# Kernel optimization log

Measured on AMD Instinct MI355X. Metric: run time of the kernel, lower is better.

## Reference

```python
import jax, jax.numpy as jnp
import numpy as np


def _segsum(x):
    """Stable segment-sum. x: (..., l) -> (..., l, l) lower-triangular sums."""
    l = x.shape[-1]
    cs = jnp.cumsum(x, axis=-1)
    seg = cs[..., :, None] - cs[..., None, :]
    mask = jnp.tril(jnp.ones((l, l), dtype=bool))
    return jnp.where(mask, seg, -jnp.inf)


def setup_inputs() -> dict:
    key = jax.random.key(0)
    kx, ka, kb, kc = jax.random.split(key, 4)
    b, s, h, p, n = 4, 8192, 32, 64, 16
    X = jax.random.normal(kx, (b, s, h, p), dtype=jnp.float32)
    # negative A for realistic decaying SSM dynamics / numerical safety
    A = -jnp.abs(jax.random.normal(ka, (b, s, h), dtype=jnp.float32)) * 0.5
    B = jax.random.normal(kb, (b, s, h, n), dtype=jnp.float32)
    C = jax.random.normal(kc, (b, s, h, n), dtype=jnp.float32)
    return {"X": X, "A": A, "B": B, "C": C, "block_len": 64}


def reference(X, A, B, C, block_len):
    b, s, h, p = X.shape
    n = B.shape[-1]
    c = s // block_len
    l = block_len
    # chunk: (b, c, l, ...)
    Xb = X.reshape(b, c, l, h, p)
    Bb = B.reshape(b, c, l, h, n)
    Cb = C.reshape(b, c, l, h, n)
    Ab = A.reshape(b, c, l, h).transpose(0, 3, 1, 2)  # (b, h, c, l)
    A_cumsum = jnp.cumsum(Ab, axis=-1)                # (b, h, c, l)

    # 1) intra-chunk (diagonal) output
    L = jnp.exp(_segsum(Ab))                          # (b, h, c, l, l)
    Y_diag = jnp.einsum("bclhn,bcshn,bhcls,bcshp->bclhp", Cb, Bb, L, Xb)

    # 2) intra-chunk states (chunk-final state contribution)
    decay_states = jnp.exp(A_cumsum[..., -1:] - A_cumsum)   # (b, h, c, l)
    states = jnp.einsum("bclhn,bhcl,bclhp->bchpn", Bb, decay_states, Xb)

    # 3) inter-chunk recurrence (zero initial states)
    A_last = A_cumsum[..., -1]                        # (b, h, c)
    decay_chunk = jnp.exp(_segsum(jnp.pad(A_last, ((0, 0), (0, 0), (1, 0)))))  # (b,h,c+1,c+1)
    states = jnp.concatenate([jnp.zeros_like(states[:, :1]), states], axis=1)  # (b,c+1,h,p,n)
    new_states = jnp.einsum("bhzc,bchpn->bzhpn", decay_chunk, states)
    states = new_states[:, :-1]                       # states entering each chunk

    # 4) state -> output (off-diagonal)
    state_decay_out = jnp.exp(A_cumsum)               # (b, h, c, l)
    Y_off = jnp.einsum("bclhn,bchpn,bhcl->bclhp", Cb, states, state_decay_out)

    Y = (Y_diag + Y_off).reshape(b, s, h, p)
    return Y
```

## Files before the change

kernel.cpp:

```cpp
#include <hip/hip_runtime.h>

#define BB 4
#define SS 8192
#define HH 32
#define PP 64
#define NN 16
#define LL 64
#define CC 128
#define SEG 4
#define NSEG (CC / SEG)
#define NCHAIN (BB * HH)
#define NSEGT (NCHAIN * NSEG)
#define NCHT (NCHAIN * CC)

typedef __attribute__((ext_vector_type(8))) short bf16x8;
typedef __attribute__((ext_vector_type(4))) short bf16x4;
typedef __attribute__((ext_vector_type(4))) float f32x4;

__device__ inline short f2bf(float f) {
    unsigned u = __builtin_bit_cast(unsigned, f);
    u = (u + 0x7FFFu + ((u >> 16) & 1u)) >> 16;
    return (short)u;
}

__global__ __launch_bounds__(256) void k1_carries(
    const float* __restrict__ X, const float* __restrict__ A,
    const float* __restrict__ B, float* __restrict__ carry,
    float* __restrict__ segd, float* __restrict__ ploc,
    float* __restrict__ dsum)
{
    int seg = blockIdx.x;
    int chain = seg >> 5;
    int kseg = seg & (NSEG - 1);
    int h = chain & (HH - 1);
    int b = chain >> 5;
    int tid = threadIdx.x;
    int w = tid >> 6, l = tid & 63, g = l >> 4, lr = l & 15;

    __shared__ float Bs[2][LL][17];
    __shared__ float csL[2][LL];
    __shared__ float wls[2][LL];

    float P[4] = {0.f, 0.f, 0.f, 0.f};
    float asum = 0.f;
    float xr[16]; float4 br; float ar = 0.f;

    int c0 = kseg * SEG;
    int pnoff = (16 * w + lr) * NN + 4 * g;

    auto LOADS = [&](int c) {
        size_t row0 = (size_t)b * SS + (size_t)c * LL;
        const float* Xp = X + (row0 * HH + h) * PP;
        const float* Bp = B + (row0 * HH + h) * NN;
        const float* Ap = A + row0 * HH + h;
#pragma unroll
        for (int kt = 0; kt < 2; ++kt)
#pragma unroll
            for (int e = 0; e < 8; ++e)
                xr[kt * 8 + e] = Xp[(size_t)(kt * 32 + g * 8 + e) * (HH * PP) + 16 * w + lr];
        br = *(const float4*)(Bp + (size_t)(tid >> 2) * (HH * NN) + (tid & 3) * 4);
        if (tid < 64) ar = Ap[(size_t)tid * HH];
    };

    auto WRITE = [&](int q1) {
        if (tid < 64) {
            float x = ar;
#pragma unroll
            for (int d = 1; d < 64; d <<= 1) {
                float t = __shfl_up(x, d, 64);
                if (tid >= d) x += t;
            }
            csL[q1][tid] = x;
            float al2 = __shfl(x, 63, 64);
            wls[q1][tid] = __expf(al2 - x);
        }
        int r = tid >> 2, qq = tid & 3;
        Bs[q1][r][qq * 4 + 0] = br.x;
        Bs[q1][r][qq * 4 + 1] = br.y;
        Bs[q1][r][qq * 4 + 2] = br.z;
        Bs[q1][r][qq * 4 + 3] = br.w;
    };

    LOADS(c0);
    WRITE(0);
    __syncthreads();

    for (int cc = 0; cc < SEG; ++cc) {
        int q = cc & 1;
        if (cc > 0) {
            float4 pv = {P[0], P[1], P[2], P[3]};
            *(float4*)(ploc + (size_t)(chain * CC + c0 + cc) * (PP * NN) + pnoff) = pv;
            if (tid == 0) dsum[chain * CC + c0 + cc] = asum;
        }
        bf16x8 xf0, xf1;
#pragma unroll
        for (int e = 0; e < 8; ++e) { xf0[e] = f2bf(xr[e]); xf1[e] = f2bf(xr[8 + e]); }
        if (cc + 1 < SEG) LOADS(c0 + cc + 1);

        bf16x8 bt[2];
#pragma unroll
        for (int kt = 0; kt < 2; ++kt) {
            bf16x8 t;
#pragma unroll
            for (int e = 0; e < 8; ++e) {
                int ll2 = kt * 32 + g * 8 + e;
                t[e] = f2bf(Bs[q][ll2][lr] * wls[q][ll2]);
            }
            bt[kt] = t;
        }
        f32x4 st = __builtin_amdgcn_mfma_f32_16x16x32_bf16(bt[0], xf0, (f32x4)0.f, 0, 0, 0);
        st = __builtin_amdgcn_mfma_f32_16x16x32_bf16(bt[1], xf1, st, 0, 0, 0);

        float alast = csL[q][LL - 1];
        float ea = __expf(alast);
#pragma unroll
        for (int r = 0; r < 4; ++r) P[r] = ea * P[r] + st[r];
        asum += alast;

        if (cc + 1 < SEG) WRITE(q ^ 1);
        __syncthreads();
    }

    float4 pv = {P[0], P[1], P[2], P[3]};
    *(float4*)(carry + (size_t)seg * (PP * NN) + pnoff) = pv;
    if (tid == 0) segd[seg] = asum;
}

__global__ __launch_bounds__(256) void k2_scan(
    const float* __restrict__ carry, const float* __restrict__ segd,
    float* __restrict__ pin)
{
    int chain = blockIdx.x >> 2;
    int t = ((blockIdx.x & 3) << 8) + threadIdx.x;
    const float* cb = carry + (size_t)chain * NSEG * (PP * NN) + t;
    float* pb = pin + (size_t)chain * NSEG * (PP * NN) + t;
    const float* as = segd + chain * NSEG;
    float P = 0.f;
    for (int k0 = 0; k0 < NSEG; k0 += 8) {
        float s[8], av[8], o[8];
#pragma unroll
        for (int u = 0; u < 8; ++u) s[u] = cb[(size_t)(k0 + u) * (PP * NN)];
#pragma unroll
        for (int u = 0; u < 8; ++u) av[u] = as[k0 + u];
#pragma unroll
        for (int u = 0; u < 8; ++u) { o[u] = P; P = __expf(av[u]) * P + s[u]; }
#pragma unroll
        for (int u = 0; u < 8; ++u) pb[(size_t)(k0 + u) * (PP * NN)] = o[u];
    }
}

__global__ __launch_bounds__(256) void k3_y(
    const float* __restrict__ X, const float* __restrict__ A,
    const float* __restrict__ Bm, const float* __restrict__ Cm,
    const float* __restrict__ pin, const float* __restrict__ ploc,
    const float* __restrict__ dsum, float* __restrict__ Y)
{
    int blk = blockIdx.x;
    int h = blk & (HH - 1);
    int c = (blk >> 5) & (CC - 1);
    int b = blk >> 12;
    int tid = threadIdx.x;
    int w = tid >> 6, l = tid & 63, g = l >> 4, lr = l & 15;
    int chain = b * HH + h;
    int seg = chain * NSEG + (c >> 2);

    __shared__ short XTF[8 * 64 * 8];
    __shared__ short ScF[8 * 64 * 8];
    __shared__ short BsF[4 * 64 * 8];
    __shared__ short PF[4 * 64 * 8];
    __shared__ float csL[LL];

    size_t row0 = (size_t)b * SS + (size_t)c * LL;
    const float* Xp = X + (row0 * HH + h) * PP;
    const float* Bp = Bm + (row0 * HH + h) * NN;
    const float* Cp = Cm + (row0 * HH + h) * NN;
    const float* Ap = A + row0 * HH + h;
    float* Yp = Y + (row0 * HH + h) * PP;

    float xr[16];
#pragma unroll
    for (int si = 0; si < 2; ++si) {
        int k0 = si * 32 + g * 8;
#pragma unroll
        for (int e = 0; e < 8; ++e)
            xr[si * 8 + e] = Xp[(size_t)(k0 + e) * (HH * PP) + 16 * w + lr];
    }
    int r = tid >> 2, q = tid & 3;
    float4 br = *(const float4*)(Bp + (size_t)r * (HH * NN) + q * 4);
    float4 cr0 = {0,0,0,0}, cr1 = {0,0,0,0};
    if (g < 2) {
        const float* crp = Cp + (size_t)(16 * w + lr) * (HH * NN) + g * 8;
        cr0 = *(const float4*)crp;
        cr1 = *(const float4*)(crp + 4);
    }
    float ar = 0.f;
    if (tid < 64) ar = Ap[(size_t)tid * HH];
    int pnoff = (16 * w + lr) * NN + 4 * g;
    float4 pinv = *(const float4*)(pin + (size_t)seg * (PP * NN) + pnoff);
    float P4[4];
    if ((c & (SEG - 1)) == 0) {
        P4[0] = pinv.x; P4[1] = pinv.y; P4[2] = pinv.z; P4[3] = pinv.w;
    } else {
        float4 plv = *(const float4*)(ploc + (size_t)(chain * CC + c) * (PP * NN) + pnoff);
        float ed = __expf(dsum[chain * CC + c]);
        P4[0] = ed * pinv.x + plv.x;
        P4[1] = ed * pinv.y + plv.y;
        P4[2] = ed * pinv.z + plv.z;
        P4[3] = ed * pinv.w + plv.w;
    }

    ((bf16x8*)ScF)[tid] = (bf16x8)0;
    ((bf16x8*)ScF)[tid + 256] = (bf16x8)0;
    if (tid < 128)
        ((bf16x8*)PF)[(tid >> 5) * 64 + 32 + (tid & 31)] = (bf16x8)0;

#pragma unroll
    for (int si = 0; si < 2; ++si) {
        bf16x8 xb;
#pragma unroll
        for (int e = 0; e < 8; ++e) xb[e] = f2bf(xr[si * 8 + e]);
        ((bf16x8*)XTF)[tid + si * 256] = xb;
    }
    {
        int fl = (r & 15) + 16 * (q >> 1);
        int jt = r >> 4;
        bf16x4 bb = { f2bf(br.x), f2bf(br.y), f2bf(br.z), f2bf(br.w) };
        ((bf16x4*)BsF)[(jt * 64 + fl) * 2 + (q & 1)] = bb;
        int zt = tid >> 6, zu = (tid >> 1) & 31, zv = tid & 1;
        ((bf16x4*)BsF)[(zt * 64 + 32 + zu) * 2 + zv] = (bf16x4)0;
    }
#pragma unroll
    for (int rr = 0; rr < 4; ++rr) {
        int n = 4 * g + rr;
        PF[(w * 64 + (n >> 3) * 16 + lr) * 8 + (n & 7)] = f2bf(P4[rr]);
    }
    bf16x8 caw = (bf16x8)0;
    if (g < 2) {
        caw[0] = f2bf(cr0.x); caw[1] = f2bf(cr0.y);
        caw[2] = f2bf(cr0.z); caw[3] = f2bf(cr0.w);
        caw[4] = f2bf(cr1.x); caw[5] = f2bf(cr1.y);
        caw[6] = f2bf(cr1.z); caw[7] = f2bf(cr1.w);
    }
    if (tid < 64) {
        float x = ar;
#pragma unroll
        for (int d = 1; d < 64; d <<= 1) {
            float t = __shfl_up(x, d, 64);
            if (tid >= d) x += t;
        }
        csL[tid] = x;
    }
    __syncthreads();

    float cs_i[4], ei[4];
    int ib = 16 * w + 4 * g;
#pragma unroll
    for (int rr = 0; rr < 4; ++rr) { cs_i[rr] = csL[ib + rr]; ei[rr] = __expf(cs_i[rr]); }

    for (int jt = 0; jt <= w; ++jt) {
        bf16x8 bw = ((bf16x8*)BsF)[jt * 64 + l];
        f32x4 sr = __builtin_amdgcn_mfma_f32_16x16x32_bf16(caw, bw, (f32x4)0.f, 0, 0, 0);
        int j = jt * 16 + lr;
        float csj = csL[j];
        int kt2 = j >> 5;
        int flb = 16 * ((j >> 3) & 3);
#pragma unroll
        for (int rr = 0; rr < 4; ++rr) {
            int i15 = g * 4 + rr;
            int i = 16 * w + i15;
            float v = (j <= i) ? sr[rr] * __expf(cs_i[rr] - csj) : 0.f;
            ScF[((w * 2 + kt2) * 64 + i15 + flb) * 8 + (j & 7)] = f2bf(v);
        }
    }

    f32x4 acc[4];
#pragma unroll
    for (int pt = 0; pt < 4; ++pt) {
        bf16x8 pfv = ((bf16x8*)PF)[pt * 64 + l];
        acc[pt] = __builtin_amdgcn_mfma_f32_16x16x32_bf16(caw, pfv, (f32x4)0.f, 0, 0, 0);
    }
#pragma unroll
    for (int pt = 0; pt < 4; ++pt)
#pragma unroll
        for (int rr = 0; rr < 4; ++rr) acc[pt][rr] *= ei[rr];

    int kts = (w >= 2) ? 2 : 1;
    for (int kt = 0; kt < kts; ++kt) {
        bf16x8 af = ((bf16x8*)ScF)[(w * 2 + kt) * 64 + l];
#pragma unroll
        for (int pt = 0; pt < 4; ++pt) {
            bf16x8 xf = ((bf16x8*)XTF)[(kt * 4 + pt) * 64 + l];
            acc[pt] = __builtin_amdgcn_mfma_f32_16x16x32_bf16(af, xf, acc[pt], 0, 0, 0);
        }
    }

#pragma unroll
    for (int pt = 0; pt < 4; ++pt)
#pragma unroll
        for (int rr = 0; rr < 4; ++rr)
            Yp[(size_t)(16 * w + 4 * g + rr) * (HH * PP) + pt * 16 + lr] = acc[pt][rr];
}

extern "C" void kernel_launch(void* const* d_in, const int* in_sizes, int n_in,
                              void* d_out, int out_size, void* d_ws, size_t ws_size,
                              hipStream_t stream)
{
    const float* X = (const float*)d_in[0];
    const float* A = (const float*)d_in[1];
    const float* B = (const float*)d_in[2];
    const float* C = (const float*)d_in[3];
    float* Y = (float*)d_out;

    float* carry = (float*)d_ws;
    float* pin   = carry + (size_t)NSEGT * (PP * NN);
    float* ploc  = pin   + (size_t)NSEGT * (PP * NN);
    float* segd  = ploc  + (size_t)NCHT * (PP * NN);
    float* dsum  = segd  + NSEGT;

    dim3 blk(256);
    k1_carries<<<dim3(NSEGT), blk, 0, stream>>>(X, A, B, carry, segd, ploc, dsum);
    k2_scan<<<dim3(NCHAIN * 4), blk, 0, stream>>>(carry, segd, pin);
    k3_y<<<dim3(NCHT), blk, 0, stream>>>(X, A, B, C, pin, ploc, dsum, Y);
}
```

Measured before the change: 275.9 us.

## Compute per-chunk states in parallel and scan all chunks in place

Replaces the segmented carry scheme (one block per 4-chunk segment, then a segment-level scan, then local-prefix fixups in the output kernel) with one block per chunk computing its own state. A scan over all 128 chunks then runs in place on the states buffer. The output kernel reads the entering state directly and replaces the shared-memory cumsum with wave shuffles. This raises parallelism in the first kernel and simplifies the third, at the cost of a longer serial scan chain (128 steps instead of 32) and more state traffic in the scan kernel.

```diff
diff --git a/kernel.cpp b/kernel.cpp
--- a/kernel.cpp
+++ b/kernel.cpp
@@ -7,10 +7,7 @@
 #define NN 16
 #define LL 64
 #define CC 128
-#define SEG 4
-#define NSEG (CC / SEG)
 #define NCHAIN (BB * HH)
-#define NSEGT (NCHAIN * NSEG)
 #define NCHT (NCHAIN * CC)
 
 typedef __attribute__((ext_vector_type(8))) short bf16x8;
@@ -23,137 +20,10 @@
     return (short)u;
 }
 
-__global__ __launch_bounds__(256) void k1_carries(
+__global__ __launch_bounds__(256) void k1_states(
     const float* __restrict__ X, const float* __restrict__ A,
-    const float* __restrict__ B, float* __restrict__ carry,
-    float* __restrict__ segd, float* __restrict__ ploc,
-    float* __restrict__ dsum)
-{
-    int seg = blockIdx.x;
-    int chain = seg >> 5;
-    int kseg = seg & (NSEG - 1);
-    int h = chain & (HH - 1);
-    int b = chain >> 5;
-    int tid = threadIdx.x;
-    int w = tid >> 6, l = tid & 63, g = l >> 4, lr = l & 15;
-
-    __shared__ float Bs[2][LL][17];
-    __shared__ float csL[2][LL];
-    __shared__ float wls[2][LL];
-
-    float P[4] = {0.f, 0.f, 0.f, 0.f};
-    float asum = 0.f;
-    float xr[16]; float4 br; float ar = 0.f;
-
-    int c0 = kseg * SEG;
-    int pnoff = (16 * w + lr) * NN + 4 * g;
-
-    auto LOADS = [&](int c) {
-        size_t row0 = (size_t)b * SS + (size_t)c * LL;
-        const float* Xp = X + (row0 * HH + h) * PP;
-        const float* Bp = B + (row0 * HH + h) * NN;
-        const float* Ap = A + row0 * HH + h;
-#pragma unroll
-        for (int kt = 0; kt < 2; ++kt)
-#pragma unroll
-            for (int e = 0; e < 8; ++e)
-                xr[kt * 8 + e] = Xp[(size_t)(kt * 32 + g * 8 + e) * (HH * PP) + 16 * w + lr];
-        br = *(const float4*)(Bp + (size_t)(tid >> 2) * (HH * NN) + (tid & 3) * 4);
-        if (tid < 64) ar = Ap[(size_t)tid * HH];
-    };
-
-    auto WRITE = [&](int q1) {
-        if (tid < 64) {
-            float x = ar;
-#pragma unroll
-            for (int d = 1; d < 64; d <<= 1) {
-                float t = __shfl_up(x, d, 64);
-                if (tid >= d) x += t;
-            }
-            csL[q1][tid] = x;
-            float al2 = __shfl(x, 63, 64);
-            wls[q1][tid] = __expf(al2 - x);
-        }
-        int r = tid >> 2, qq = tid & 3;
-        Bs[q1][r][qq * 4 + 0] = br.x;
-        Bs[q1][r][qq * 4 + 1] = br.y;
-        Bs[q1][r][qq * 4 + 2] = br.z;
-        Bs[q1][r][qq * 4 + 3] = br.w;
-    };
-
-    LOADS(c0);
-    WRITE(0);
-    __syncthreads();
-
-    for (int cc = 0; cc < SEG; ++cc) {
-        int q = cc & 1;
-        if (cc > 0) {
-            float4 pv = {P[0], P[1], P[2], P[3]};
-            *(float4*)(ploc + (size_t)(chain * CC + c0 + cc) * (PP * NN) + pnoff) = pv;
-            if (tid == 0) dsum[chain * CC + c0 + cc] = asum;
-        }
-        bf16x8 xf0, xf1;
-#pragma unroll
-        for (int e = 0; e < 8; ++e) { xf0[e] = f2bf(xr[e]); xf1[e] = f2bf(xr[8 + e]); }
-        if (cc + 1 < SEG) LOADS(c0 + cc + 1);
-
-        bf16x8 bt[2];
-#pragma unroll
-        for (int kt = 0; kt < 2; ++kt) {
-            bf16x8 t;
-#pragma unroll
-            for (int e = 0; e < 8; ++e) {
-                int ll2 = kt * 32 + g * 8 + e;
-                t[e] = f2bf(Bs[q][ll2][lr] * wls[q][ll2]);
-            }
-            bt[kt] = t;
-        }
-        f32x4 st = __builtin_amdgcn_mfma_f32_16x16x32_bf16(bt[0], xf0, (f32x4)0.f, 0, 0, 0);
-        st = __builtin_amdgcn_mfma_f32_16x16x32_bf16(bt[1], xf1, st, 0, 0, 0);
-
-        float alast = csL[q][LL - 1];
-        float ea = __expf(alast);
-#pragma unroll
-        for (int r = 0; r < 4; ++r) P[r] = ea * P[r] + st[r];
-        asum += alast;
-
-        if (cc + 1 < SEG) WRITE(q ^ 1);
-        __syncthreads();
-    }
-
-    float4 pv = {P[0], P[1], P[2], P[3]};
-    *(float4*)(carry + (size_t)seg * (PP * NN) + pnoff) = pv;
-    if (tid == 0) segd[seg] = asum;
-}
-
-__global__ __launch_bounds__(256) void k2_scan(
-    const float* __restrict__ carry, const float* __restrict__ segd,
-    float* __restrict__ pin)
-{
-    int chain = blockIdx.x >> 2;
-    int t = ((blockIdx.x & 3) << 8) + threadIdx.x;
-    const float* cb = carry + (size_t)chain * NSEG * (PP * NN) + t;
-    float* pb = pin + (size_t)chain * NSEG * (PP * NN) + t;
-    const float* as = segd + chain * NSEG;
-    float P = 0.f;
-    for (int k0 = 0; k0 < NSEG; k0 += 8) {
-        float s[8], av[8], o[8];
-#pragma unroll
-        for (int u = 0; u < 8; ++u) s[u] = cb[(size_t)(k0 + u) * (PP * NN)];
-#pragma unroll
-        for (int u = 0; u < 8; ++u) av[u] = as[k0 + u];
-#pragma unroll
-        for (int u = 0; u < 8; ++u) { o[u] = P; P = __expf(av[u]) * P + s[u]; }
-#pragma unroll
-        for (int u = 0; u < 8; ++u) pb[(size_t)(k0 + u) * (PP * NN)] = o[u];
-    }
-}
-
-__global__ __launch_bounds__(256) void k3_y(
-    const float* __restrict__ X, const float* __restrict__ A,
-    const float* __restrict__ Bm, const float* __restrict__ Cm,
-    const float* __restrict__ pin, const float* __restrict__ ploc,
-    const float* __restrict__ dsum, float* __restrict__ Y)
+    const float* __restrict__ B, float* __restrict__ states,
+    float* __restrict__ alast_g)
 {
     int blk = blockIdx.x;
     int h = blk & (HH - 1);
@@ -162,13 +32,96 @@
     int tid = threadIdx.x;
     int w = tid >> 6, l = tid & 63, g = l >> 4, lr = l & 15;
     int chain = b * HH + h;
-    int seg = chain * NSEG + (c >> 2);
+
+    __shared__ float Bs[LL][17];
+
+    size_t row0 = (size_t)b * SS + (size_t)c * LL;
+    const float* Xp = X + (row0 * HH + h) * PP;
+    const float* Bp = B + (row0 * HH + h) * NN;
+    const float* Ap = A + row0 * HH + h;
+
+    float av = Ap[(size_t)l * HH];
+    int r = tid >> 2, q = tid & 3;
+    float4 br = *(const float4*)(Bp + (size_t)r * (HH * NN) + q * 4);
+    float xr[16];
+#pragma unroll
+    for (int kt = 0; kt < 2; ++kt)
+#pragma unroll
+        for (int e = 0; e < 8; ++e)
+            xr[kt * 8 + e] = Xp[(size_t)(kt * 32 + g * 8 + e) * (HH * PP) + 16 * w + lr];
+
+    float x = av;
+#pragma unroll
+    for (int d = 1; d < 64; d <<= 1) {
+        float t = __shfl_up(x, d, 64);
+        if (l >= d) x += t;
+    }
+    float alast = __shfl(x, 63, 64);
+
+    float wlr = __expf(alast - __shfl(x, r & 63, 64));
+    Bs[r][q * 4 + 0] = br.x * wlr;
+    Bs[r][q * 4 + 1] = br.y * wlr;
+    Bs[r][q * 4 + 2] = br.z * wlr;
+    Bs[r][q * 4 + 3] = br.w * wlr;
+    __syncthreads();
+
+    bf16x8 bt[2], xf[2];
+#pragma unroll
+    for (int kt = 0; kt < 2; ++kt)
+#pragma unroll
+        for (int e = 0; e < 8; ++e) {
+            int row = kt * 32 + g * 8 + e;
+            bt[kt][e] = f2bf(Bs[row][lr]);
+            xf[kt][e] = f2bf(xr[kt * 8 + e]);
+        }
+    f32x4 st = __builtin_amdgcn_mfma_f32_16x16x32_bf16(bt[0], xf[0], (f32x4)0.f, 0, 0, 0);
+    st = __builtin_amdgcn_mfma_f32_16x16x32_bf16(bt[1], xf[1], st, 0, 0, 0);
+
+    float4 pv = {st[0], st[1], st[2], st[3]};
+    *(float4*)(states + (size_t)(chain * CC + c) * (PP * NN) + (16 * w + lr) * NN + 4 * g) = pv;
+    if (tid == 0) alast_g[chain * CC + c] = alast;
+}
+
+__global__ __launch_bounds__(256) void k2_scan(
+    float* __restrict__ states, const float* __restrict__ alast_g)
+{
+    int chain = blockIdx.x >> 2;
+    int t = ((blockIdx.x & 3) << 8) + threadIdx.x;
+    __shared__ float eal[CC];
+    if (threadIdx.x < CC)
+        eal[threadIdx.x] = __expf(alast_g[chain * CC + threadIdx.x]);
+    __syncthreads();
+
+    float* base = states + (size_t)chain * CC * (PP * NN) + t;
+    float P = 0.f;
+    for (int c0 = 0; c0 < CC; c0 += 8) {
+        float s[8], o[8];
+#pragma unroll
+        for (int u = 0; u < 8; ++u) s[u] = base[(size_t)(c0 + u) * (PP * NN)];
+#pragma unroll
+        for (int u = 0; u < 8; ++u) { o[u] = P; P = eal[c0 + u] * P + s[u]; }
+#pragma unroll
+        for (int u = 0; u < 8; ++u) base[(size_t)(c0 + u) * (PP * NN)] = o[u];
+    }
+}
+
+__global__ __launch_bounds__(256) void k3_y(
+    const float* __restrict__ X, const float* __restrict__ A,
+    const float* __restrict__ Bm, const float* __restrict__ Cm,
+    const float* __restrict__ pin, float* __restrict__ Y)
+{
+    int blk = blockIdx.x;
+    int h = blk & (HH - 1);
+    int c = (blk >> 5) & (CC - 1);
+    int b = blk >> 12;
+    int tid = threadIdx.x;
+    int w = tid >> 6, l = tid & 63, g = l >> 4, lr = l & 15;
+    int chain = b * HH + h;
 
     __shared__ short XTF[8 * 64 * 8];
     __shared__ short ScF[8 * 64 * 8];
     __shared__ short BsF[4 * 64 * 8];
     __shared__ short PF[4 * 64 * 8];
-    __shared__ float csL[LL];
 
     size_t row0 = (size_t)b * SS + (size_t)c * LL;
     const float* Xp = X + (row0 * HH + h) * PP;
@@ -177,14 +130,7 @@
     const float* Ap = A + row0 * HH + h;
     float* Yp = Y + (row0 * HH + h) * PP;
 
-    float xr[16];
-#pragma unroll
-    for (int si = 0; si < 2; ++si) {
-        int k0 = si * 32 + g * 8;
-#pragma unroll
-        for (int e = 0; e < 8; ++e)
-            xr[si * 8 + e] = Xp[(size_t)(k0 + e) * (HH * PP) + 16 * w + lr];
-    }
+    float av = Ap[(size_t)l * HH];
     int r = tid >> 2, q = tid & 3;
     float4 br = *(const float4*)(Bp + (size_t)r * (HH * NN) + q * 4);
     float4 cr0 = {0,0,0,0}, cr1 = {0,0,0,0};
@@ -193,34 +139,34 @@
         cr0 = *(const float4*)crp;
         cr1 = *(const float4*)(crp + 4);
     }
-    float ar = 0.f;
-    if (tid < 64) ar = Ap[(size_t)tid * HH];
-    int pnoff = (16 * w + lr) * NN + 4 * g;
-    float4 pinv = *(const float4*)(pin + (size_t)seg * (PP * NN) + pnoff);
-    float P4[4];
-    if ((c & (SEG - 1)) == 0) {
-        P4[0] = pinv.x; P4[1] = pinv.y; P4[2] = pinv.z; P4[3] = pinv.w;
-    } else {
-        float4 plv = *(const float4*)(ploc + (size_t)(chain * CC + c) * (PP * NN) + pnoff);
-        float ed = __expf(dsum[chain * CC + c]);
-        P4[0] = ed * pinv.x + plv.x;
-        P4[1] = ed * pinv.y + plv.y;
-        P4[2] = ed * pinv.z + plv.z;
-        P4[3] = ed * pinv.w + plv.w;
+    float4 pinv = *(const float4*)(pin + (size_t)(chain * CC + c) * (PP * NN) + (16 * w + lr) * NN + 4 * g);
+    float xr[16];
+#pragma unroll
+    for (int si = 0; si < 2; ++si) {
+        int k0 = si * 32 + g * 8;
+#pragma unroll
+        for (int e = 0; e < 8; ++e)
+            xr[si * 8 + e] = Xp[(size_t)(k0 + e) * (HH * PP) + 16 * w + lr];
+    }
+
+    float x = av;
+#pragma unroll
+    for (int d = 1; d < 64; d <<= 1) {
+        float t = __shfl_up(x, d, 64);
+        if (l >= d) x += t;
+    }
+    float cs_i[4], ei[4];
+    int ib = 16 * w + 4 * g;
+#pragma unroll
+    for (int rr = 0; rr < 4; ++rr) {
+        cs_i[rr] = __shfl(x, ib + rr, 64);
+        ei[rr] = __expf(cs_i[rr]);
     }
 
     ((bf16x8*)ScF)[tid] = (bf16x8)0;
     ((bf16x8*)ScF)[tid + 256] = (bf16x8)0;
     if (tid < 128)
         ((bf16x8*)PF)[(tid >> 5) * 64 + 32 + (tid & 31)] = (bf16x8)0;
-
-#pragma unroll
-    for (int si = 0; si < 2; ++si) {
-        bf16x8 xb;
-#pragma unroll
-        for (int e = 0; e < 8; ++e) xb[e] = f2bf(xr[si * 8 + e]);
-        ((bf16x8*)XTF)[tid + si * 256] = xb;
-    }
     {
         int fl = (r & 15) + 16 * (q >> 1);
         int jt = r >> 4;
@@ -229,10 +175,13 @@
         int zt = tid >> 6, zu = (tid >> 1) & 31, zv = tid & 1;
         ((bf16x4*)BsF)[(zt * 64 + 32 + zu) * 2 + zv] = (bf16x4)0;
     }
-#pragma unroll
-    for (int rr = 0; rr < 4; ++rr) {
-        int n = 4 * g + rr;
-        PF[(w * 64 + (n >> 3) * 16 + lr) * 8 + (n & 7)] = f2bf(P4[rr]);
+    {
+        float P4[4] = {pinv.x, pinv.y, pinv.z, pinv.w};
+#pragma unroll
+        for (int rr = 0; rr < 4; ++rr) {
+            int n = 4 * g + rr;
+            PF[(w * 64 + (n >> 3) * 16 + lr) * 8 + (n & 7)] = f2bf(P4[rr]);
+        }
     }
     bf16x8 caw = (bf16x8)0;
     if (g < 2) {
@@ -241,27 +190,24 @@
         caw[4] = f2bf(cr1.x); caw[5] = f2bf(cr1.y);
         caw[6] = f2bf(cr1.z); caw[7] = f2bf(cr1.w);
     }
-    if (tid < 64) {
-        float x = ar;
-#pragma unroll
-        for (int d = 1; d < 64; d <<= 1) {
-            float t = __shfl_up(x, d, 64);
-            if (tid >= d) x += t;
-        }
-        csL[tid] = x;
-    }
-    __syncthreads();
-
-    float cs_i[4], ei[4];
-    int ib = 16 * w + 4 * g;
-#pragma unroll
-    for (int rr = 0; rr < 4; ++rr) { cs_i[rr] = csL[ib + rr]; ei[rr] = __expf(cs_i[rr]); }
+    __syncthreads();
+
+    f32x4 acc[4];
+#pragma unroll
+    for (int pt = 0; pt < 4; ++pt) {
+        bf16x8 pfv = ((bf16x8*)PF)[pt * 64 + l];
+        acc[pt] = __builtin_amdgcn_mfma_f32_16x16x32_bf16(caw, pfv, (f32x4)0.f, 0, 0, 0);
+    }
+#pragma unroll
+    for (int pt = 0; pt < 4; ++pt)
+#pragma unroll
+        for (int rr = 0; rr < 4; ++rr) acc[pt][rr] *= ei[rr];
 
     for (int jt = 0; jt <= w; ++jt) {
         bf16x8 bw = ((bf16x8*)BsF)[jt * 64 + l];
         f32x4 sr = __builtin_amdgcn_mfma_f32_16x16x32_bf16(caw, bw, (f32x4)0.f, 0, 0, 0);
         int j = jt * 16 + lr;
-        float csj = csL[j];
+        float csj = __shfl(x, j, 64);
         int kt2 = j >> 5;
         int flb = 16 * ((j >> 3) & 3);
 #pragma unroll
@@ -273,16 +219,14 @@
         }
     }
 
-    f32x4 acc[4];
-#pragma unroll
-    for (int pt = 0; pt < 4; ++pt) {
-        bf16x8 pfv = ((bf16x8*)PF)[pt * 64 + l];
-        acc[pt] = __builtin_amdgcn_mfma_f32_16x16x32_bf16(caw, pfv, (f32x4)0.f, 0, 0, 0);
-    }
-#pragma unroll
-    for (int pt = 0; pt < 4; ++pt)
-#pragma unroll
-        for (int rr = 0; rr < 4; ++rr) acc[pt][rr] *= ei[rr];
+#pragma unroll
+    for (int si = 0; si < 2; ++si) {
+        bf16x8 xb;
+#pragma unroll
+        for (int e = 0; e < 8; ++e) xb[e] = f2bf(xr[si * 8 + e]);
+        ((bf16x8*)XTF)[tid + si * 256] = xb;
+    }
+    __syncthreads();
 
     int kts = (w >= 2) ? 2 : 1;
     for (int kt = 0; kt < kts; ++kt) {
@@ -311,14 +255,11 @@
     const float* C = (const float*)d_in[3];
     float* Y = (float*)d_out;
 
-    float* carry = (float*)d_ws;
-    float* pin   = carry + (size_t)NSEGT * (PP * NN);
-    float* ploc  = pin   + (size_t)NSEGT * (PP * NN);
-    float* segd  = ploc  + (size_t)NCHT * (PP * NN);
-    float* dsum  = segd  + NSEGT;
+    float* states = (float*)d_ws;
+    float* alast  = states + (size_t)NCHT * (PP * NN);
 
     dim3 blk(256);
-    k1_carries<<<dim3(NSEGT), blk, 0, stream>>>(X, A, B, carry, segd, ploc, dsum);
-    k2_scan<<<dim3(NCHAIN * 4), blk, 0, stream>>>(carry, segd, pin);
-    k3_y<<<dim3(NCHT), blk, 0, stream>>>(X, A, B, C, pin, ploc, dsum, Y);
-}
+    k1_states<<<dim3(NCHT), blk, 0, stream>>>(X, A, B, states, alast);
+    k2_scan<<<dim3(NCHAIN * 4), blk, 0, stream>>>(states, alast);
+    k3_y<<<dim3(NCHT), blk, 0, stream>>>(X, A, B, C, states, Y);
+}
```

After: 276.3 us. Within noise of the previous version (+0.2%).
